# Kernel optimization log

Measured on AMD Instinct MI355X. Metric: run time of the kernel, lower is better.

Reference implementation:

```python
import jax, jax.numpy as jnp
import numpy as np

B, C, H, W = 8, 64, 32, 32
NEG = 256
TEMP = 2.0
FACTOR = 0.8
EPS = 1e-8


def setup_inputs() -> dict:
    key = jax.random.key(0)
    k1, k2, k3, k4 = jax.random.split(key, 4)
    views_1 = jax.random.normal(k1, (B, C, H, W), dtype=jnp.float32)
    views_2 = jax.random.normal(k2, (B, C, H, W), dtype=jnp.float32)
    img = jax.random.uniform(k3, (1, 3, H, W), dtype=jnp.float32)
    neg_idx = jax.random.randint(k4, (B, 2, H * W, NEG), 0, H, dtype=jnp.int32)
    return {"views_1": views_1, "views_2": views_2, "img": img, "neg_idx": neg_idx}


def _forward(views_1, views_2, img, neg_idx):
    hw = H * W
    height = jnp.arange(hw) // W
    width = jnp.arange(hw) % W
    coords = jnp.stack([height, width]).astype(jnp.float32)  # [2, hw]
    img0 = img[0]  # [3, H, W]; original uses img[0] for EVERY batch element
    euc_norm = jnp.sqrt(jnp.asarray((H - 1) ** 2 + (W - 1) ** 2, jnp.float32))
    sqrt3 = jnp.sqrt(jnp.asarray(3.0, jnp.float32))

    center = img0[:, height, width]  # [3, hw]

    def per_sample(z1, z2, nidx):
        # nidx: [2, hw, neg]
        nf = nidx.astype(jnp.float32)
        # torch.norm with no dim => scalar Frobenius norm over [2, neg] per pixel
        d = coords[:, :, None] - nf  # [2, hw, neg]
        euc = jnp.sqrt(jnp.sum(d * d, axis=(0, 2))) / euc_norm  # [hw]
        negs = img0[:, nidx[0], nidx[1]]  # [3, hw, neg]
        rd = center[:, :, None] - negs
        rgb = jnp.sqrt(jnp.sum(rd * rd, axis=(0, 2))) / sqrt3  # [hw]
        weight = euc * FACTOR + rgb * (1.0 - FACTOR)  # [hw], constant across neg

        z1v = z1.reshape(C, hw)  # [c, hw]
        pn = z2[:, nidx[0], nidx[1]]  # [c, hw, neg]
        dot = jnp.einsum('cp,cpn->pn', z1v, pn)  # [hw, neg]
        z1sq = jnp.sum(z1v * z1v, axis=0)  # [hw]
        z1n = jnp.sqrt(z1sq)
        pnn = jnp.sqrt(jnp.sum(pn * pn, axis=0))  # [hw, neg]
        cos = dot / jnp.maximum(z1n[:, None] * pnn, EPS)  # [hw, neg]
        cos0 = z1sq / jnp.maximum(z1sq, EPS)  # [hw] (self-similarity ~ 1)

        sim_neg = jnp.minimum(jnp.abs(cos * weight[:, None]), 1.0)  # [hw, neg]
        sim0 = jnp.minimum(jnp.abs(cos0), 1.0)  # [hw]
        sim = jnp.concatenate(
            [jnp.mean(sim0)[None], jnp.mean(sim_neg, axis=0) / TEMP]
        )  # [neg+1]

        # BCELoss with target = [1, 0, ..., 0]; torch clamps log terms at -100
        logp = jnp.maximum(jnp.log(sim[0]), -100.0)
        log1m = jnp.maximum(jnp.log1p(-sim[1:]), -100.0)
        bce = -(logp + jnp.sum(log1m)) / (NEG + 1)
        return bce, sim

    bce, sims = jax.vmap(per_sample)(views_1, views_2, neg_idx)
    loss = jnp.mean(bce)
    sim_all = jnp.sum(sims, axis=0)
    return (loss, sim_all[0] / B, jnp.sum(sim_all[1:]) / NEG * TEMP / B)


def reference(views_1, views_2, img, neg_idx):
    return _forward(views_1, views_2, img, neg_idx)
```

## Files before the change

### kernel.cpp

```cpp
#include <hip/hip_runtime.h>
#include <math.h>

#define BB 8
#define CC 64
#define HH 32
#define WW 32
#define HW 1024
#define NEGN 256
#define TEMP 2.0f
#define FACTOR 0.8f
#define EPSF 1e-8f

typedef short bf16x8 __attribute__((ext_vector_type(8)));
typedef float f32x4  __attribute__((ext_vector_type(4)));

__device__ inline unsigned short f2bf(float f) {
    unsigned u = __float_as_uint(f);
    u += 0x7FFFu + ((u >> 16) & 1u);
    return (unsigned short)(u >> 16);
}


__global__ __launch_bounds__(256) void prep_z2(
    const float* __restrict__ z2,
    unsigned short* __restrict__ z2t,
    float* __restrict__ normq_ws)
{
    __shared__ float ctile[64 * 16];

    const int t   = threadIdx.x;
    const int blk = blockIdx.x;
    const int b   = blk >> 6;
    const int q0  = (blk & 63) * 16;

    #pragma unroll
    for (int i = 0; i < 4; ++i) {
        const int idx = t + 256 * i;
        const int c = idx >> 4, row = idx & 15;
        ctile[idx] = z2[((size_t)(b * CC + c)) * HW + q0 + row];
    }
    __syncthreads();

    if (t < 16) {
        float s = 0.f;
        #pragma unroll
        for (int c = 0; c < CC; ++c) { const float v = ctile[c * 16 + t]; s += v * v; }
        normq_ws[b * 1024 + q0 + t] = sqrtf(s);
    }

    unsigned short* dst = z2t + ((size_t)(b * 1024) + q0) * 64;
    ushort4 pk;
    const int o = 4 * t;
    pk.x = f2bf(ctile[((o + 0) & 63) * 16 + ((o + 0) >> 6)]);
    pk.y = f2bf(ctile[((o + 1) & 63) * 16 + ((o + 1) >> 6)]);
    pk.z = f2bf(ctile[((o + 2) & 63) * 16 + ((o + 2) >> 6)]);
    pk.w = f2bf(ctile[((o + 3) & 63) * 16 + ((o + 3) >> 6)]);
    *reinterpret_cast<ushort4*>(dst + o) = pk;
}

__global__ __launch_bounds__(256, 2) void gemm_fused(
    const float* __restrict__ z1,
    const float* __restrict__ img,
    const int*   __restrict__ nidx,
    const unsigned short* __restrict__ z2t,
    const float* __restrict__ normq_ws,
    float* __restrict__ simPart,
    float* __restrict__ sim0Part)
{
    __shared__ float Dt_s[16 * HW];
    __shared__ float aux[3 * HW];
    __shared__ float z1n_s[16];
    __shared__ float z1sq_s[16];

    const int t    = threadIdx.x;
    const int blk  = blockIdx.x;
    const int b    = blk >> 6;
    const int p0   = (blk & 63) * 16;
    const int wave = t >> 6;
    const int lane = t & 63;
    const int ln15 = lane & 15;
    const int lg   = lane >> 4;

    const int p_b = t >> 4;
    const int tn  = t & 15;
    const size_t nbase = ((size_t)(b * 2) * HW + p0 + p_b) * NEGN;
    const int2* __restrict__ nr = reinterpret_cast<const int2*>(nidx + nbase);
    const int2* __restrict__ nc =
        reinterpret_cast<const int2*>(nidx + nbase + (size_t)HW * NEGN);
    int2 rrv[8], ccv[8];
    #pragma unroll
    for (int j = 0; j < 8; ++j) {
        rrv[j] = nr[tn + 16 * j];
        ccv[j] = nc[tn + 16 * j];
    }

    float* nq_s  = aux;
    float* ctile = aux + HW;
    reinterpret_cast<float4*>(nq_s)[t] =
        reinterpret_cast<const float4*>(normq_ws + b * 1024)[t];
    #pragma unroll
    for (int i = 0; i < 4; ++i) {
        const int idx = t + 256 * i;
        const int c = idx >> 4, row = idx & 15;
        ctile[idx] = z1[((size_t)(b * CC + c)) * HW + p0 + row];
    }
    __syncthreads();

    if (t < 16) {
        float s = 0.f;
        #pragma unroll
        for (int c = 0; c < CC; ++c) { const float v = ctile[c * 16 + t]; s += v * v; }
        z1sq_s[t] = s; z1n_s[t] = sqrtf(s);
    }
    bf16x8 a0, a1;
    #pragma unroll
    for (int j = 0; j < 8; ++j) {
        a0[j] = (short)f2bf(ctile[(lg * 8 + j) * 16 + ln15]);
        a1[j] = (short)f2bf(ctile[(32 + lg * 8 + j) * 16 + ln15]);
    }
    __syncthreads();

    const int qw = wave * 256;
    #pragma unroll 4
    for (int tile = 0; tile < 16; ++tile) {
        const int q0t = qw + tile * 16;
        const unsigned short* brow =
            z2t + ((size_t)(b * 1024) + q0t + ln15) * 64 + lg * 8;
        const bf16x8 b0 = *reinterpret_cast<const bf16x8*>(brow);
        const bf16x8 b1 = *reinterpret_cast<const bf16x8*>(brow + 32);
        f32x4 acc = {0.f, 0.f, 0.f, 0.f};
        acc = __builtin_amdgcn_mfma_f32_16x16x32_bf16(a0, b0, acc, 0, 0, 0);
        acc = __builtin_amdgcn_mfma_f32_16x16x32_bf16(a1, b1, acc, 0, 0, 0);

        const float pn = nq_s[q0t + ln15];
        #pragma unroll
        for (int i = 0; i < 4; ++i) {
            const int row = lg * 4 + i;
            Dt_s[row * HW + q0t + ln15] = acc[i] / fmaxf(z1n_s[row] * pn, EPSF);
        }
    }
    __syncthreads();

    {
        const float4* __restrict__ imgf4 = reinterpret_cast<const float4*>(img);
        float4* imgs4 = reinterpret_cast<float4*>(aux);
        #pragma unroll
        for (int j = 0; j < 3; ++j) imgs4[t + 256 * j] = imgf4[t + 256 * j];
    }
    __syncthreads();
    float* imgs_l = aux;

    const int pg = p0 + p_b;
    const float cen0 = imgs_l[pg], cen1 = imgs_l[HW + pg], cen2 = imgs_l[2 * HW + pg];
    const float hp = (float)(pg >> 5), wp = (float)(pg & 31);

    int qv[16];
    float se = 0.f, sr = 0.f;
    #pragma unroll
    for (int j = 0; j < 8; ++j) {
        {
            const int q = rrv[j].x * WW + ccv[j].x; qv[2 * j] = q;
            const float dh = hp - (float)rrv[j].x, dw = wp - (float)ccv[j].x;
            se += dh * dh + dw * dw;
            const float d0 = cen0 - imgs_l[q];
            const float d1 = cen1 - imgs_l[HW + q];
            const float d2 = cen2 - imgs_l[2 * HW + q];
            sr += d0 * d0 + d1 * d1 + d2 * d2;
        }
        {
            const int q = rrv[j].y * WW + ccv[j].y; qv[2 * j + 1] = q;
            const float dh = hp - (float)rrv[j].y, dw = wp - (float)ccv[j].y;
            se += dh * dh + dw * dw;
            const float d0 = cen0 - imgs_l[q];
            const float d1 = cen1 - imgs_l[HW + q];
            const float d2 = cen2 - imgs_l[2 * HW + q];
            sr += d0 * d0 + d1 * d1 + d2 * d2;
        }
    }
    #pragma unroll
    for (int off = 8; off; off >>= 1) {
        se += __shfl_xor(se, off);
        sr += __shfl_xor(sr, off);
    }
    const float euc_norm = sqrtf((float)((HH - 1) * (HH - 1) + (WW - 1) * (WW - 1)));
    const float weight = sqrtf(se) / euc_norm * FACTOR +
                         sqrtf(sr) / sqrtf(3.0f) * (1.0f - FACTOR);

    float2 sv[8];
    #pragma unroll
    for (int j = 0; j < 8; ++j) {
        const float c0 = Dt_s[p_b * HW + qv[2 * j]];
        const float c1 = Dt_s[p_b * HW + qv[2 * j + 1]];
        sv[j].x = fminf(fabsf(c0 * weight), 1.0f);
        sv[j].y = fminf(fabsf(c1 * weight), 1.0f);
    }
    __syncthreads();

    float2* simpart2 = reinterpret_cast<float2*>(Dt_s);
    #pragma unroll
    for (int j = 0; j < 8; ++j)
        simpart2[p_b * (NEGN / 2) + tn + 16 * j] = sv[j];
    __syncthreads();

    float s = 0.f;
    #pragma unroll
    for (int pp = 0; pp < 16; ++pp) s += Dt_s[pp * NEGN + t];
    simPart[(size_t)blk * NEGN + t] = s;

    if (t == 0) {
        float s0 = 0.f;
        #pragma unroll
        for (int pp = 0; pp < 16; ++pp)
            s0 += fminf(fabsf(z1sq_s[pp] / fmaxf(z1sq_s[pp], EPSF)), 1.0f);
        sim0Part[blk] = s0;
    }
}

__global__ __launch_bounds__(256) void reduce_out(
    const float* __restrict__ simPart,
    const float* __restrict__ sim0Part,
    float* __restrict__ out)
{
    const int b = blockIdx.x;
    const int t = threadIdx.x;

    float a = 0.f;
    #pragma unroll 8
    for (int pblk = 0; pblk < 64; ++pblk)
        a += simPart[((size_t)(b * 64 + pblk)) * NEGN + t];

    const float s = a * (1.0f / HW) * (1.0f / TEMP);
    float ssum = s;
    float lsum = fmaxf(log1pf(-s), -100.0f);

    __shared__ float rs[4], rl[4];
    __shared__ float s0sh;
    #pragma unroll
    for (int off = 32; off; off >>= 1) {
        ssum += __shfl_down(ssum, off);
        lsum += __shfl_down(lsum, off);
    }
    if ((t & 63) == 0) { rs[t >> 6] = ssum; rl[t >> 6] = lsum; }

    if (t < 64) {
        float v = sim0Part[b * 64 + t];
        #pragma unroll
        for (int off = 32; off; off >>= 1) v += __shfl_xor(v, off);
        if (t == 0) s0sh = v * (1.0f / HW);
    }
    __syncthreads();

    if (t == 0) {
        const float S = rs[0] + rs[1] + rs[2] + rs[3];
        const float L = rl[0] + rl[1] + rl[2] + rl[3];
        const float s0 = s0sh;
        const float logp = fmaxf(logf(s0), -100.0f);
        atomicAdd(out + 0, -(logp + L) / ((float)(NEGN + 1) * (float)BB));
        atomicAdd(out + 1, s0 / (float)BB);
        atomicAdd(out + 2, S / (float)NEGN * TEMP / (float)BB);
    }
}

extern "C" void kernel_launch(void* const* d_in, const int* in_sizes, int n_in,
                              void* d_out, int out_size, void* d_ws, size_t ws_size,
                              hipStream_t stream) {
    const float* v1   = (const float*)d_in[0];
    const float* v2   = (const float*)d_in[1];
    const float* img  = (const float*)d_in[2];
    const int*   nidx = (const int*)  d_in[3];

    float*    simPart  = (float*)d_ws;
    float*    sim0Part = simPart + 512 * NEGN;
    float*    normq_ws = sim0Part + 512;
    unsigned short* z2t = (unsigned short*)(normq_ws + 8192);

    prep_z2<<<512, 256, 0, stream>>>(v2, z2t, normq_ws);
    gemm_fused<<<512, 256, 0, stream>>>(v1, img, nidx, z2t, normq_ws,
                                        simPart, sim0Part);
    reduce_out<<<BB, 256, 0, stream>>>(simPart, sim0Part, (float*)d_out);
}
```

Measured before the change: 89.76 us.

## Load z1 tile straight into registers and overlap image staging with GEMM

Each lane now loads its z1 A-operand values directly from global memory into registers and computes the row norms with cross-lane shuffles, so the shared-memory ctile staging is gone. The per-column norms are held in registers instead of shared memory. The image is copied into its own shared buffer at kernel start, which lets the image/weight computation run before a single barrier instead of after the GEMM. This drops two or three __syncthreads and some LDS traffic. In exchange it uses more registers and makes strided, uncoalesced global loads of z1.

```diff
diff --git a/kernel.cpp b/kernel.cpp
--- a/kernel.cpp
+++ b/kernel.cpp
@@ -68,8 +68,7 @@
     float* __restrict__ sim0Part)
 {
     __shared__ float Dt_s[16 * HW];
-    __shared__ float aux[3 * HW];
-    __shared__ float z1n_s[16];
+    __shared__ float imgs_l[3 * HW];
     __shared__ float z1sq_s[16];
 
     const int t    = threadIdx.x;
@@ -94,33 +93,48 @@
         ccv[j] = nc[tn + 16 * j];
     }
 
-    float* nq_s  = aux;
-    float* ctile = aux + HW;
-    reinterpret_cast<float4*>(nq_s)[t] =
-        reinterpret_cast<const float4*>(normq_ws + b * 1024)[t];
-    #pragma unroll
-    for (int i = 0; i < 4; ++i) {
-        const int idx = t + 256 * i;
-        const int c = idx >> 4, row = idx & 15;
-        ctile[idx] = z1[((size_t)(b * CC + c)) * HW + p0 + row];
-    }
-    __syncthreads();
-
-    if (t < 16) {
-        float s = 0.f;
-        #pragma unroll
-        for (int c = 0; c < CC; ++c) { const float v = ctile[c * 16 + t]; s += v * v; }
-        z1sq_s[t] = s; z1n_s[t] = sqrtf(s);
-    }
+    {
+        const float4* __restrict__ imgf4 = reinterpret_cast<const float4*>(img);
+        float4* imgs4 = reinterpret_cast<float4*>(imgs_l);
+        #pragma unroll
+        for (int j = 0; j < 3; ++j) imgs4[t + 256 * j] = imgf4[t + 256 * j];
+    }
+
+    const int qw = wave * 256;
+    float pnv[16];
+    #pragma unroll
+    for (int tile = 0; tile < 16; ++tile)
+        pnv[tile] = normq_ws[b * 1024 + qw + tile * 16 + ln15];
+
+    const float* __restrict__ z1p = z1 + (size_t)(b * CC) * HW + p0 + ln15;
+    float av0[8], av1[8];
+    #pragma unroll
+    for (int j = 0; j < 8; ++j) {
+        av0[j] = z1p[(size_t)(lg * 8 + j) * HW];
+        av1[j] = z1p[(size_t)(32 + lg * 8 + j) * HW];
+    }
+    float zsq = 0.f;
+    #pragma unroll
+    for (int j = 0; j < 8; ++j) zsq += av0[j] * av0[j];
+    #pragma unroll
+    for (int j = 0; j < 8; ++j) zsq += av1[j] * av1[j];
+    zsq += __shfl_xor(zsq, 16);
+    zsq += __shfl_xor(zsq, 32);
+    const float z1n_mine = sqrtf(zsq);
+    float z1n_row[4];
+    #pragma unroll
+    for (int i = 0; i < 4; ++i) z1n_row[i] = __shfl(z1n_mine, lg * 4 + i);
+
     bf16x8 a0, a1;
     #pragma unroll
     for (int j = 0; j < 8; ++j) {
-        a0[j] = (short)f2bf(ctile[(lg * 8 + j) * 16 + ln15]);
-        a1[j] = (short)f2bf(ctile[(32 + lg * 8 + j) * 16 + ln15]);
-    }
-    __syncthreads();
-
-    const int qw = wave * 256;
+        a0[j] = (short)f2bf(av0[j]);
+        a1[j] = (short)f2bf(av1[j]);
+    }
+    if (wave == 0 && lane < 16) z1sq_s[lane] = zsq;
+
+    __syncthreads();
+
     #pragma unroll 4
     for (int tile = 0; tile < 16; ++tile) {
         const int q0t = qw + tile * 16;
@@ -131,24 +145,13 @@
         f32x4 acc = {0.f, 0.f, 0.f, 0.f};
         acc = __builtin_amdgcn_mfma_f32_16x16x32_bf16(a0, b0, acc, 0, 0, 0);
         acc = __builtin_amdgcn_mfma_f32_16x16x32_bf16(a1, b1, acc, 0, 0, 0);
-
-        const float pn = nq_s[q0t + ln15];
         #pragma unroll
         for (int i = 0; i < 4; ++i) {
             const int row = lg * 4 + i;
-            Dt_s[row * HW + q0t + ln15] = acc[i] / fmaxf(z1n_s[row] * pn, EPSF);
+            Dt_s[row * HW + q0t + ln15] =
+                acc[i] / fmaxf(z1n_row[i] * pnv[tile], EPSF);
         }
     }
-    __syncthreads();
-
-    {
-        const float4* __restrict__ imgf4 = reinterpret_cast<const float4*>(img);
-        float4* imgs4 = reinterpret_cast<float4*>(aux);
-        #pragma unroll
-        for (int j = 0; j < 3; ++j) imgs4[t + 256 * j] = imgf4[t + 256 * j];
-    }
-    __syncthreads();
-    float* imgs_l = aux;
 
     const int pg = p0 + p_b;
     const float cen0 = imgs_l[pg], cen1 = imgs_l[HW + pg], cen2 = imgs_l[2 * HW + pg];
@@ -186,6 +189,8 @@
     const float weight = sqrtf(se) / euc_norm * FACTOR +
                          sqrtf(sr) / sqrtf(3.0f) * (1.0f - FACTOR);
 
+    __syncthreads();
+
     float2 sv[8];
     #pragma unroll
     for (int j = 0; j < 8; ++j) {
```

Measured after the change: 90.87 us. Within noise of the previous version (+1.2%).
